# Optimization experiments

Hardware: AMD Instinct MI355X
Metric: run time of the kernel (lower is better)

The kernel has to match this reference:

```python
import jax, jax.numpy as jnp
import numpy as np
from jax import lax

B, T, I, H = 128, 48, 128, 512


def setup_inputs() -> dict:
    key = jax.random.key(0)
    ks = jax.random.split(key, 16)
    s = lambda *sh: 1.0 / np.sqrt(sh[-1])
    inp = {
        "decoder_x": jax.random.normal(ks[0], (B, T, I), jnp.float32),
        "x": jax.random.normal(ks[1], (B, T, 3), jnp.float32),
        # xavier_normal for [num_layers=1, B, H] -> std = sqrt(2/(B+H))
        "h0": jax.random.normal(ks[2], (B, H), jnp.float32) * np.sqrt(2.0 / (B + H)),
        "W1": jax.random.normal(ks[3], (H, H), jnp.float32) * s(H),
        "b1": jnp.zeros((H,), jnp.float32),
        "W2": jax.random.normal(ks[4], (H, I), jnp.float32) * s(I),
        "b2": jnp.zeros((H,), jnp.float32),
        "W3": jax.random.normal(ks[5], (1, H), jnp.float32) * s(H),
        "b3": jnp.zeros((1,), jnp.float32),
        "W4": jax.random.normal(ks[6], (H, I + 3), jnp.float32) * s(I + 3),
        "b4": jnp.zeros((H,), jnp.float32),
        "W_ih": jax.random.normal(ks[7], (3 * H, H), jnp.float32) * s(H),
        "W_hh": jax.random.normal(ks[8], (3 * H, H), jnp.float32) * s(H),
        "b_ih": jnp.zeros((3 * H,), jnp.float32),
        "b_hh": jnp.zeros((3 * H,), jnp.float32),
        "Wfc": jax.random.normal(ks[9], (1, H), jnp.float32) * s(H),
        "bfc": jnp.zeros((1,), jnp.float32),
    }
    return inp


def reference(decoder_x, x, h0, W1, b1, W2, b2, W3, b3, W4, b4,
              W_ih, W_hh, b_ih, b_hh, Wfc, bfc):
    Bc, Tc, Ic = decoder_x.shape
    # layer2(decoder_x) is step-invariant: compute once. [B, T, H]
    w2 = jnp.einsum('bti,hi->bth', decoder_x, W2) + b2

    def step(carry, x_t):
        h, _ = carry  # h: [B, H]
        w1 = h @ W1.T + b1                              # [B, H]
        # attention energies over the T_1 encoder window
        e = jnp.tanh(w1[:, None, :] + w2) @ W3[0] + b3[0]   # [B, T]
        a = jax.nn.softmax(e, axis=1)                   # [B, T]
        c = jnp.einsum('bti,bt->bi', decoder_x, a)      # weighted context [B, I]
        y0 = jnp.concatenate([c, x_t], axis=1) @ W4.T + b4  # [B, H]
        # single-step GRU (PyTorch gate order r, z, n)
        gi = y0 @ W_ih.T + b_ih
        gh = h @ W_hh.T + b_hh
        ir, iz, in_ = jnp.split(gi, 3, axis=1)
        hr, hz, hn = jnp.split(gh, 3, axis=1)
        r = jax.nn.sigmoid(ir + hr)
        z = jax.nn.sigmoid(iz + hz)
        n = jnp.tanh(in_ + r * hn)
        h_new = (1.0 - z) * n + z * h
        return (h_new, a), None

    xs = jnp.swapaxes(x, 0, 1)  # [T, B, 3]
    (h_f, a_f), _ = lax.scan(step, (h0, jnp.zeros((Bc, Tc), decoder_x.dtype)), xs)
    re = h_f @ Wfc.T + bfc      # fc(final_output[:, -1, :])  -> [B, 1]
    return re, a_f[:, :, None]  # weighted_alpha from last step [B, T, 1]
```

## Files before the change

### kernel.cpp

```cpp
#include <hip/hip_runtime.h>


typedef _Float16 half8 __attribute__((ext_vector_type(8)));
typedef _Float16 h2v  __attribute__((ext_vector_type(2)));
typedef float    f32x4 __attribute__((ext_vector_type(4)));
typedef unsigned int u32x3 __attribute__((ext_vector_type(3)));

#define OFF_BAR   0u
#define OFF_BZ    32768u
#define OFF_BC    40960u
#define OFF_WZ    65536u
#define OFF_WCT   2162688u
#define OFF_W2H   3178496u
#define OFF_HGH   9732096u
#define OFF_ZG    9863168u
#define OFF_DW    10911744u

__device__ __forceinline__ float fexp2(float x) { return __builtin_amdgcn_exp2f(x); }
__device__ __forceinline__ float frcp(float x)  { return __builtin_amdgcn_rcpf(x); }
__device__ __forceinline__ float fast_tanh(float x) {
  x = fminf(fmaxf(x, -15.f), 15.f);
  float e = fexp2(x * 2.8853900817779268f);
  return (e - 1.f) * frcp(e + 1.f);
}
__device__ __forceinline__ float fast_sigmoid(float x) {
  x = fminf(fmaxf(x, -30.f), 30.f);
  float e = fexp2(x * 1.4426950408889634f);
  return e * frcp(e + 1.f);
}

__device__ __forceinline__ void st_f32(float* p, float v) {
  __hip_atomic_store(p, v, __ATOMIC_RELAXED, __HIP_MEMORY_SCOPE_AGENT);
}
__device__ __forceinline__ unsigned long long ld_u64(const void* p) {
  return __hip_atomic_load((const unsigned long long*)p, __ATOMIC_RELAXED,
                           __HIP_MEMORY_SCOPE_AGENT);
}
__device__ __forceinline__ void st_u32(unsigned int* p, unsigned int v) {
  __hip_atomic_store(p, v, __ATOMIC_RELAXED, __HIP_MEMORY_SCOPE_AGENT);
}
union U2 { unsigned long long u; float f[2]; };
union H4 { unsigned long long u; _Float16 h[4]; };
union HU { unsigned int u; h2v h; };

__device__ __forceinline__ void poll_ge(unsigned int* fp, bool active,
                                        unsigned int target) {
  for (;;) {
    unsigned int v = active
      ? __hip_atomic_load(fp, __ATOMIC_RELAXED, __HIP_MEMORY_SCOPE_AGENT)
      : target;
    if (__ballot(v < target) == 0) break;
    __builtin_amdgcn_s_sleep(1);
  }
  __asm__ __volatile__("" ::: "memory");
}

__global__ __launch_bounds__(256) void prep_all(
    const float* __restrict__ dx, const float* __restrict__ h0,
    const float* __restrict__ W1, const float* __restrict__ Whh,
    const float* __restrict__ b1, const float* __restrict__ bhh,
    const float* __restrict__ Wih, const float* __restrict__ W4,
    const float* __restrict__ b4, const float* __restrict__ bih,
    const float* __restrict__ W2, const float* __restrict__ b2,
    _Float16* __restrict__ hgh,
    _Float16* __restrict__ Wzh, float* __restrict__ bz,
    float* __restrict__ bc, _Float16* __restrict__ WcT,
    _Float16* __restrict__ w2h, unsigned int* __restrict__ bar)
{
  __shared__ __align__(16) char smem[58368];
  const int bid = blockIdx.x;
  const int tid = threadIdx.x;
  const int lane = tid & 63, wv = tid >> 6;

  if (bid == 0) {
    for (int i = tid; i < 8192; i += 256) bar[i] = 0u;
  } else if (bid == 1) {
    for (int n = tid; n < 2048; n += 256)
      bz[n] = (n < 512) ? b1[n] : bhh[n - 512];
  } else if (bid < 18) {
    const int o0 = (bid - 2) * 96 + wv * 24;
    for (int it = 0; it < 24; ++it) {
      const int row = o0 + it;
      const float* r = Wih + row * 512 + lane * 8;
      float s = 0.f;
#pragma unroll
      for (int u = 0; u < 8; ++u) s += r[u] * b4[lane * 8 + u];
#pragma unroll
      for (int off = 32; off >= 1; off >>= 1) s += __shfl_xor(s, off);
      if (lane == 0) bc[row] = bih[row] + s;
    }
  } else if (bid < 34) {
    const int i0 = (bid - 18) * 4096 + tid * 16;
#pragma unroll
    for (int u = 0; u < 4; ++u) {
      float4 v = *(const float4*)(h0 + i0 + u * 4);
      H4 p; p.h[0] = (_Float16)v.x; p.h[1] = (_Float16)v.y;
      p.h[2] = (_Float16)v.z; p.h[3] = (_Float16)v.w;
      *(unsigned long long*)(hgh + i0 + u * 4) = p.u;
    }
  } else if (bid < 98) {
    const int i0 = (bid - 34) * 16384 + tid * 64;
#pragma unroll 4
    for (int u = 0; u < 16; ++u) {
      const int i = i0 + u * 4;
      const float* src = (i < 262144) ? (W1 + i) : (Whh + i - 262144);
      float4 v = *(const float4*)src;
      H4 p; p.h[0] = (_Float16)v.x; p.h[1] = (_Float16)v.y;
      p.h[2] = (_Float16)v.z; p.h[3] = (_Float16)v.w;
      *(unsigned long long*)(Wzh + i) = p.u;
    }
  } else if (bid < 194) {
    float* wih = (float*)smem;
    float* w4s = (float*)(smem + 4224);
    const int o0 = (bid - 98) * 16;
    const int k = tid;
    float acc[16];
#pragma unroll
    for (int i = 0; i < 16; ++i) acc[i] = 0.f;
    for (int jc = 0; jc < 512; jc += 64) {
      __syncthreads();
      for (int idx = tid; idx < 16 * 64; idx += 256) {
        int oo = idx >> 6, jj = idx & 63;
        wih[oo * 66 + jj] = Wih[(o0 + oo) * 512 + jc + jj];
      }
      for (int idx = tid; idx < 64 * 131; idx += 256) {
        int r = idx / 131, c = idx - r * 131;
        w4s[r * 132 + c] = W4[(jc + r) * 131 + c];
      }
      __syncthreads();
      if (k < 131) {
        for (int jj = 0; jj < 64; ++jj) {
          float w4v = w4s[jj * 132 + k];
#pragma unroll
          for (int oo = 0; oo < 16; ++oo) acc[oo] += wih[oo * 66 + jj] * w4v;
        }
      }
    }
    if (k < 131) {
#pragma unroll
      for (int oo = 0; oo < 16; ++oo)
        WcT[k * 1536 + o0 + oo] = (_Float16)acc[oo];
    }
  } else {
    float* dxa = (float*)smem;
    _Float16* w2t = (_Float16*)(smem + 24576);
    const int b = bid - 194;
    for (int idx = tid; idx < 48 * 128; idx += 256)
      dxa[idx] = dx[b * 6144 + idx];
    for (int hc = 0; hc < 4; ++hc) {
      __syncthreads();
      for (int idx = tid; idx < 128 * 128; idx += 256) {
        int hl = idx >> 7, i = idx & 127;
        w2t[i * 132 + hl] = (_Float16)W2[(hc * 128 + hl) * 128 + i];
      }
      __syncthreads();
      const int hh = tid & 127;
      const int tq = tid >> 7;
      const float b2v = b2[hc * 128 + hh];
      for (int tt = tq * 24; tt < tq * 24 + 24; ++tt) {
        float acc = b2v;
#pragma unroll 4
        for (int i = 0; i < 128; ++i)
          acc += dxa[tt * 128 + i] * (float)w2t[i * 132 + hh];
        w2h[(b * 48 + tt) * 512 + hc * 128 + hh] = (_Float16)acc;
      }
    }
  }
}

__global__ __launch_bounds__(256) void prep_dw(
    const float* __restrict__ dx, const _Float16* __restrict__ WcT,
    unsigned int* __restrict__ DW12)
{
  __shared__ float dxu[16 * 128];
  const int j = blockIdx.x;
  const int tid = threadIdx.x;
  const int u0 = j * 16;
  const float4* src = (const float4*)(dx + (size_t)u0 * 128);
  float4* dst4 = (float4*)dxu;
  for (int i = tid; i < 512; i += 256) dst4[i] = src[i];
  __syncthreads();
  const int c0 = tid * 2;
  float acc[16][6];
#pragma unroll
  for (int u = 0; u < 16; ++u)
#pragma unroll
    for (int g = 0; g < 6; ++g) acc[u][g] = 0.f;
  for (int k = 0; k < 128; ++k) {
    const _Float16* wr = WcT + k * 1536 + c0;
    h2v w0 = *(const h2v*)(wr);
    h2v w1v = *(const h2v*)(wr + 512);
    h2v w2v = *(const h2v*)(wr + 1024);
    const float f0 = (float)w0[0],  f1 = (float)w0[1];
    const float f2 = (float)w1v[0], f3 = (float)w1v[1];
    const float f4 = (float)w2v[0], f5 = (float)w2v[1];
#pragma unroll
    for (int u = 0; u < 16; ++u) {
      const float d = dxu[u * 128 + k];
      acc[u][0] += d * f0; acc[u][1] += d * f1; acc[u][2] += d * f2;
      acc[u][3] += d * f3; acc[u][4] += d * f4; acc[u][5] += d * f5;
    }
  }
#pragma unroll
  for (int u = 0; u < 16; ++u) {
    unsigned int* o = DW12 + (size_t)(u0 + u) * 768 + tid * 3;
    HU p;
    p.h[0] = (_Float16)acc[u][0]; p.h[1] = (_Float16)acc[u][1]; o[0] = p.u;
    p.h[0] = (_Float16)acc[u][2]; p.h[1] = (_Float16)acc[u][3]; o[1] = p.u;
    p.h[0] = (_Float16)acc[u][4]; p.h[1] = (_Float16)acc[u][5]; o[2] = p.u;
  }
}

#define DW_STEP(TB, CUR)                                                     \
  do {                                                                       \
    _Pragma("unroll")                                                        \
    for (int j = 0; j < 4; ++j) {                                            \
      const float a = asx[(TB) * 4 + j];                                     \
      HU p0, p1, p2; p0.u = CUR[j].x; p1.u = CUR[j].y; p2.u = CUR[j].z;      \
      aR0 += a * (float)p0.h[0]; aR1 += a * (float)p0.h[1];                  \
      aZ0 += a * (float)p1.h[0]; aZ1 += a * (float)p1.h[1];                  \
      aN0 += a * (float)p2.h[0]; aN1 += a * (float)p2.h[1];                  \
    }                                                                        \
    if ((TB) < 9) {                                                          \
      _Pragma("unroll")                                                      \
      for (int j = 0; j < 4; ++j)                                            \
        CUR[j] = *(const u32x3*)(dwp + (size_t)(((TB) + 3) * 4 + j) * 768);  \
    }                                                                        \
  } while (0)

__global__ __launch_bounds__(256, 1) void decoder_main(
    const float* __restrict__ xin, const float* __restrict__ h0,
    const float* __restrict__ W3, const float* __restrict__ b3,
    const float* __restrict__ Wfc, const float* __restrict__ bfc,
    const _Float16* __restrict__ Wzh, const float* __restrict__ bz,
    const _Float16* __restrict__ WcT, const float* __restrict__ bc,
    const _Float16* __restrict__ w2h, const unsigned int* __restrict__ DW12,
    _Float16* __restrict__ hgh, float* __restrict__ zg,
    unsigned int* __restrict__ bar, float* __restrict__ out)
{
  const int tid  = threadIdx.x;
  const int lane = tid & 63;
  const int wv   = tid >> 6;
  const int bid  = blockIdx.x;
  const int grp  = bid & 7;
  const int mem  = bid >> 3;
  const int b0   = grp * 16;
  const int myrow = b0 + mem;
  const int cb   = mem * 128;
  const int myIdx = grp * 16 + mem;
  const int base16 = grp * 16;
  unsigned int* zflag = bar;
  unsigned int* hflag = bar + 4096;

  __shared__ __align__(16) _Float16 w2lds[48 * 512];
  __shared__ __align__(16) char hlds[16384];
  __shared__ __align__(16) unsigned int dwlds[24 * 768];
  __shared__ float xlds[48 * 4];
  __shared__ float wfcs[512];
  __shared__ float es[48];
  __shared__ float asx[48];
  __shared__ float red[4];

  const int m = lane & 15, q = lane >> 4;

  half8 wzf[2][16];
  int   ncol[2];
  float bzv[2];
#pragma unroll
  for (int t = 0; t < 2; ++t) {
    ncol[t] = cb + (wv * 2 + t) * 16 + m;
    const _Float16* wrow = Wzh + ncol[t] * 512 + q * 8;
#pragma unroll
    for (int ks = 0; ks < 16; ++ks)
      wzf[t][ks] = *(const half8*)(wrow + ks * 32);
    bzv[t] = bz[ncol[t]];
  }
  float w3r[8];
#pragma unroll
  for (int u = 0; u < 8; ++u) w3r[u] = W3[lane * 8 + u];
  const float b3v  = b3[0];
  const float bfcv = bfc[0];

  const int c0 = tid * 2;
  const float bcR0 = bc[c0],        bcR1 = bc[c0 + 1];
  const float bcZ0 = bc[512 + c0],  bcZ1 = bc[513 + c0];
  const float bcN0 = bc[1024 + c0], bcN1 = bc[1025 + c0];
  float wxR[3][2], wxZ[3][2], wxN[3][2];
#pragma unroll
  for (int j2 = 0; j2 < 3; ++j2) {
    const _Float16* wr = WcT + (128 + j2) * 1536 + c0;
    wxR[j2][0] = (float)wr[0];    wxR[j2][1] = (float)wr[1];
    wxZ[j2][0] = (float)wr[512];  wxZ[j2][1] = (float)wr[513];
    wxN[j2][0] = (float)wr[1024]; wxN[j2][1] = (float)wr[1025];
  }
  float hA = h0[myrow * 512 + c0];
  float hB = h0[myrow * 512 + c0 + 1];

  const float* __restrict__ zrow = zg + (size_t)myrow * 2048;
  const unsigned int* __restrict__ dwp =
      DW12 + (size_t)myrow * 48 * 768 + (size_t)tid * 3;

  {
    const half8* w2src = (const half8*)(w2h + (size_t)myrow * 48 * 512);
    half8* w2dst = (half8*)w2lds;
    for (int i = tid; i < 3072; i += 256) w2dst[i] = w2src[i];
    for (int i = tid; i < 512; i += 256) wfcs[i] = Wfc[i];
    for (int i = tid; i < 144; i += 256) {
      const int t = i / 3, j2 = i - t * 3;
      xlds[t * 4 + j2] = xin[myrow * 144 + i];
    }
    const unsigned int* dwsrc = DW12 + (size_t)myrow * 48 * 768;
    for (int i = tid; i < 24 * 256; i += 256) {
      u32x3 v = *(const u32x3*)(dwsrc + (size_t)i * 3);
      *(u32x3*)(dwlds + (size_t)i * 3) = v;
    }
  }
  __syncthreads();

  for (int step = 0; step < 48; ++step) {
    {
      poll_ge(hflag + (size_t)(b0 + wv * 4 + (lane & 3)) * 32, lane < 4,
              (unsigned int)step);
      unsigned long long hv[8];
      const char* hbase = (const char*)hgh + (size_t)b0 * 1024 + (size_t)wv * 4096;
#pragma unroll
      for (int u = 0; u < 8; ++u)
        hv[u] = ld_u64(hbase + (size_t)(u * 64 + lane) * 8);
#pragma unroll
      for (int u = 0; u < 8; ++u) {
        const int n = wv * 512 + u * 64 + lane;
        const int row = n >> 7, b8 = (n & 127) * 8;
        *(unsigned long long*)(hlds + row * 1024 + (b8 ^ ((row & 7) << 4))) = hv[u];
      }
    }
    __syncthreads();

    {
      half8 af[16];
      const char* hb = hlds + m * 1024;
      const int sw = (m & 7) << 4;
#pragma unroll
      for (int ks = 0; ks < 16; ++ks)
        af[ks] = *(const half8*)(hb + ((ks * 64 + q * 16) ^ sw));
#pragma unroll
      for (int t = 0; t < 2; ++t) {
        f32x4 acc = {bzv[t], bzv[t], bzv[t], bzv[t]};
#pragma unroll
        for (int ks = 0; ks < 16; ++ks)
          acc = __builtin_amdgcn_mfma_f32_16x16x32_f16(af[ks], wzf[t][ks], acc, 0, 0, 0);
#pragma unroll
        for (int r = 0; r < 4; ++r)
          st_f32(&zg[(size_t)(b0 + q * 4 + r) * 2048 + ncol[t]], acc[r]);
      }
    }
    __syncthreads();
    if (tid == 0) st_u32(&zflag[(size_t)myIdx * 32], (unsigned int)(step + 1));

    poll_ge(zflag + (size_t)(base16 + (lane & 15)) * 32, lane < 16,
            (unsigned int)(step + 1));

    float w1r[8];
    {
#pragma unroll
      for (int u2 = 0; u2 < 4; ++u2) {
        U2 t2; t2.u = ld_u64(zrow + lane * 8 + u2 * 2);
        w1r[u2 * 2] = t2.f[0]; w1r[u2 * 2 + 1] = t2.f[1];
      }
    }
    U2 tr, tz, tn2;
    tr.u  = ld_u64(zrow + 512 + c0);
    tz.u  = ld_u64(zrow + 1024 + c0);
    tn2.u = ld_u64(zrow + 1536 + c0);
    u32x3 bA[4], bB[4], bC[4];
#pragma unroll
    for (int j = 0; j < 4; ++j) bA[j] = *(const u32x3*)(dwp + (size_t)(24 + j) * 768);
#pragma unroll
    for (int j = 0; j < 4; ++j) bB[j] = *(const u32x3*)(dwp + (size_t)(28 + j) * 768);
#pragma unroll
    for (int j = 0; j < 4; ++j) bC[j] = *(const u32x3*)(dwp + (size_t)(32 + j) * 768);

    {
      for (int tt = 0; tt < 12; ++tt) {
        const int t = wv * 12 + tt;
        half8 w2v = *(const half8*)(w2lds + t * 512 + lane * 8);
        float p = 0.f;
#pragma unroll
        for (int u = 0; u < 8; ++u)
          p += w3r[u] * fast_tanh(w1r[u] + (float)w2v[u]);
#pragma unroll
        for (int off = 32; off >= 1; off >>= 1) p += __shfl_xor(p, off);
        if (lane == 0) es[t] = p + b3v;
      }
      __syncthreads();
      if (wv == 0) {
        float e = (lane < 48) ? es[lane] : -1e30f;
        float mx = e;
#pragma unroll
        for (int off = 32; off >= 1; off >>= 1) mx = fmaxf(mx, __shfl_xor(mx, off));
        float pe = (lane < 48) ? fexp2((e - mx) * 1.4426950408889634f) : 0.f;
        float s = pe;
#pragma unroll
        for (int off = 32; off >= 1; off >>= 1) s += __shfl_xor(s, off);
        float a = pe * frcp(s);
        if (lane < 48) {
          asx[lane] = a;
          if (step == 47) out[128 + myrow * 48 + lane] = a;
        }
      }
      __syncthreads();
    }

    {
      float aR0 = bcR0, aR1 = bcR1, aZ0 = bcZ0, aZ1 = bcZ1, aN0 = bcN0, aN1 = bcN1;
#pragma unroll 4
      for (int t = 0; t < 24; ++t) {
        const float a = asx[t];
        u32x3 d = *(const u32x3*)(dwlds + (size_t)(t * 256 + tid) * 3);
        HU p0, p1, p2; p0.u = d.x; p1.u = d.y; p2.u = d.z;
        aR0 += a * (float)p0.h[0]; aR1 += a * (float)p0.h[1];
        aZ0 += a * (float)p1.h[0]; aZ1 += a * (float)p1.h[1];
        aN0 += a * (float)p2.h[0]; aN1 += a * (float)p2.h[1];
      }
      DW_STEP(6, bA);  DW_STEP(7, bB);  DW_STEP(8, bC);
      DW_STEP(9, bA);  DW_STEP(10, bB); DW_STEP(11, bC);

      const float x0 = xlds[step * 4], x1 = xlds[step * 4 + 1], x2 = xlds[step * 4 + 2];
      aR0 += x0 * wxR[0][0] + x1 * wxR[1][0] + x2 * wxR[2][0];
      aR1 += x0 * wxR[0][1] + x1 * wxR[1][1] + x2 * wxR[2][1];
      aZ0 += x0 * wxZ[0][0] + x1 * wxZ[1][0] + x2 * wxZ[2][0];
      aZ1 += x0 * wxZ[0][1] + x1 * wxZ[1][1] + x2 * wxZ[2][1];
      aN0 += x0 * wxN[0][0] + x1 * wxN[1][0] + x2 * wxN[2][0];
      aN1 += x0 * wxN[0][1] + x1 * wxN[1][1] + x2 * wxN[2][1];

      const float r0 = fast_sigmoid(aR0 + tr.f[0]), r1 = fast_sigmoid(aR1 + tr.f[1]);
      const float z0 = fast_sigmoid(aZ0 + tz.f[0]), z1 = fast_sigmoid(aZ1 + tz.f[1]);
      const float n0 = fast_tanh(aN0 + r0 * tn2.f[0]), n1 = fast_tanh(aN1 + r1 * tn2.f[1]);
      hA = (1.f - z0) * n0 + z0 * hA;
      hB = (1.f - z1) * n1 + z1 * hB;
      HU hp; hp.h[0] = (_Float16)hA; hp.h[1] = (_Float16)hB;
      st_u32((unsigned int*)(hgh + myrow * 512 + c0), hp.u);
    }
    __syncthreads();
    if (tid == 0) st_u32(&hflag[(size_t)myrow * 32], (unsigned int)(step + 1));
  }

  {
    float p = hA * wfcs[c0] + hB * wfcs[c0 + 1];
#pragma unroll
    for (int off = 32; off >= 1; off >>= 1) p += __shfl_xor(p, off);
    if (lane == 0) red[wv] = p;
    __syncthreads();
    if (tid == 0) out[myrow] = red[0] + red[1] + red[2] + red[3] + bfcv;
  }
}

extern "C" void kernel_launch(void* const* d_in, const int* in_sizes, int n_in,
                              void* d_out, int out_size, void* d_ws, size_t ws_size,
                              hipStream_t stream) {
  (void)in_sizes; (void)n_in; (void)out_size; (void)ws_size;
  const float* dx  = (const float*)d_in[0];
  const float* xin = (const float*)d_in[1];
  const float* h0  = (const float*)d_in[2];
  const float* W1  = (const float*)d_in[3];
  const float* b1  = (const float*)d_in[4];
  const float* W2  = (const float*)d_in[5];
  const float* b2  = (const float*)d_in[6];
  const float* W3  = (const float*)d_in[7];
  const float* b3  = (const float*)d_in[8];
  const float* W4  = (const float*)d_in[9];
  const float* b4  = (const float*)d_in[10];
  const float* Wih = (const float*)d_in[11];
  const float* Whh = (const float*)d_in[12];
  const float* bih = (const float*)d_in[13];
  const float* bhh = (const float*)d_in[14];
  const float* Wfc = (const float*)d_in[15];
  const float* bfc = (const float*)d_in[16];

  char* ws = (char*)d_ws;
  unsigned int* bar = (unsigned int*)(ws + OFF_BAR);
  float*     bz  = (float*)(ws + OFF_BZ);
  float*     bc  = (float*)(ws + OFF_BC);
  _Float16*  Wzh = (_Float16*)(ws + OFF_WZ);
  _Float16*  WcT = (_Float16*)(ws + OFF_WCT);
  _Float16*  w2h = (_Float16*)(ws + OFF_W2H);
  _Float16*  hgh = (_Float16*)(ws + OFF_HGH);
  float*     zg  = (float*)(ws + OFF_ZG);
  unsigned int* DW12 = (unsigned int*)(ws + OFF_DW);

  prep_all<<<322, 256, 0, stream>>>(dx, h0, W1, Whh, b1, bhh, Wih, W4, b4, bih,
                                    W2, b2, hgh, Wzh, bz, bc, WcT, w2h, bar);
  prep_dw<<<384, 256, 0, stream>>>(dx, WcT, DW12);
  decoder_main<<<128, 256, 0, stream>>>(xin, h0, W3, b3, Wfc, bfc,
                                        Wzh, bz, WcT, bc, w2h, DW12,
                                        hgh, zg, bar, (float*)d_out);
}
```

Before: 882.6 us.

## Use sc0 inline-asm loads and stores for inter-block flag and state exchange

After: 1.188 ms. +34.6%, slower.

```diff
diff --git a/kernel.cpp b/kernel.cpp
--- a/kernel.cpp
+++ b/kernel.cpp
@@ -43,12 +43,39 @@
 union H4 { unsigned long long u; _Float16 h[4]; };
 union HU { unsigned int u; h2v h; };
 
+__device__ __forceinline__ unsigned int ld_flag_sc0(const unsigned int* p) {
+  unsigned int v;
+  asm volatile("global_load_dword %0, %1, off sc0\n\t"
+               "s_waitcnt vmcnt(0)"
+               : "=v"(v) : "v"(p) : "memory");
+  return v;
+}
+__device__ __forceinline__ void st_u32_sc0(unsigned int* p, unsigned int v) {
+  asm volatile("global_store_dword %0, %1, off sc0" :: "v"(p), "v"(v) : "memory");
+}
+__device__ __forceinline__ void st_f32_sc0(float* p, float v) {
+  asm volatile("global_store_dword %0, %1, off sc0" :: "v"(p), "v"(v) : "memory");
+}
+__device__ __forceinline__ void drain_vm() {
+  asm volatile("s_waitcnt vmcnt(0)" ::: "memory");
+  __builtin_amdgcn_sched_barrier(0);
+}
+
 __device__ __forceinline__ void poll_ge(unsigned int* fp, bool active,
                                         unsigned int target) {
   for (;;) {
     unsigned int v = active
       ? __hip_atomic_load(fp, __ATOMIC_RELAXED, __HIP_MEMORY_SCOPE_AGENT)
       : target;
+    if (__ballot(v < target) == 0) break;
+    __builtin_amdgcn_s_sleep(1);
+  }
+  __asm__ __volatile__("" ::: "memory");
+}
+__device__ __forceinline__ void poll_ge_sc0(const unsigned int* fp,
+                                            unsigned int target) {
+  for (;;) {
+    unsigned int v = ld_flag_sc0(fp);
     if (__ballot(v < target) == 0) break;
     __builtin_amdgcn_s_sleep(1);
   }
@@ -260,8 +287,41 @@
   __shared__ float es[48];
   __shared__ float asx[48];
   __shared__ float red[4];
+  __shared__ unsigned int probe_sh;
 
   const int m = lane & 15, q = lane >> 4;
+
+  bool fast;
+  {
+    if (wv == 0) {
+      bool okr[2];
+#pragma unroll
+      for (int r = 1; r <= 2; ++r) {
+        if (lane == 0)
+          st_u32_sc0(zflag + (size_t)myIdx * 32 + 16, (unsigned int)r);
+        const unsigned int* pp = zflag + (size_t)(base16 + (lane & 15)) * 32 + 16;
+        bool ok = false;
+        for (int it = 0; it < 1000 && !ok; ++it) {
+          unsigned int v = ld_flag_sc0(pp);
+          if (__ballot(v < (unsigned int)r) == 0) ok = true;
+          else __builtin_amdgcn_s_sleep(8);
+        }
+        if (lane == 0)
+          st_u32(zflag + (size_t)myIdx * 32 + 16 + r, ok ? 2u : 1u);
+        unsigned int* vp = zflag + (size_t)(base16 + (lane & 15)) * 32 + 16 + r;
+        unsigned int v;
+        for (;;) {
+          v = __hip_atomic_load(vp, __ATOMIC_RELAXED, __HIP_MEMORY_SCOPE_AGENT);
+          if (__ballot(v == 0u) == 0) break;
+          __builtin_amdgcn_s_sleep(1);
+        }
+        okr[r - 1] = (__ballot(v == 2u) == ~0ull);
+      }
+      if (lane == 0) probe_sh = (okr[0] && okr[1]) ? 1u : 0u;
+    }
+    __syncthreads();
+    fast = (probe_sh != 0u);
+  }
 
   half8 wzf[2][16];
   int   ncol[2];
@@ -319,18 +379,42 @@
 
   for (int step = 0; step < 48; ++step) {
     {
-      poll_ge(hflag + (size_t)(b0 + wv * 4 + (lane & 3)) * 32, lane < 4,
-              (unsigned int)step);
-      unsigned long long hv[8];
-      const char* hbase = (const char*)hgh + (size_t)b0 * 1024 + (size_t)wv * 4096;
-#pragma unroll
-      for (int u = 0; u < 8; ++u)
-        hv[u] = ld_u64(hbase + (size_t)(u * 64 + lane) * 8);
-#pragma unroll
-      for (int u = 0; u < 8; ++u) {
-        const int n = wv * 512 + u * 64 + lane;
-        const int row = n >> 7, b8 = (n & 127) * 8;
-        *(unsigned long long*)(hlds + row * 1024 + (b8 ^ ((row & 7) << 4))) = hv[u];
+      if (fast) {
+        poll_ge_sc0(hflag + (size_t)(b0 + wv * 4 + (lane & 3)) * 32,
+                    (unsigned int)step);
+        f32x4 hv4[4];
+        const char* ab = (const char*)hgh + (size_t)b0 * 1024 +
+                         (size_t)wv * 4096 + (size_t)lane * 16;
+        asm volatile(
+          "global_load_dwordx4 %0, %4, off sc0\n\t"
+          "global_load_dwordx4 %1, %4, off offset:1024 sc0\n\t"
+          "global_load_dwordx4 %2, %4, off offset:2048 sc0\n\t"
+          "global_load_dwordx4 %3, %4, off offset:3072 sc0\n\t"
+          "s_waitcnt vmcnt(0)"
+          : "=v"(hv4[0]), "=v"(hv4[1]), "=v"(hv4[2]), "=v"(hv4[3])
+          : "v"(ab) : "memory");
+#pragma unroll
+        for (int v2 = 0; v2 < 4; ++v2) {
+          const int c = v2 * 64 + lane;
+          const int n0 = wv * 512 + c * 2;
+          const int row = n0 >> 7;
+          const int x = (n0 & 127) * 8;
+          *(f32x4*)(hlds + row * 1024 + (x ^ ((row & 7) << 4))) = hv4[v2];
+        }
+      } else {
+        poll_ge(hflag + (size_t)(b0 + wv * 4 + (lane & 3)) * 32, lane < 4,
+                (unsigned int)step);
+        unsigned long long hv[8];
+        const char* hbase = (const char*)hgh + (size_t)b0 * 1024 + (size_t)wv * 4096;
+#pragma unroll
+        for (int u = 0; u < 8; ++u)
+          hv[u] = ld_u64(hbase + (size_t)(u * 64 + lane) * 8);
+#pragma unroll
+        for (int u = 0; u < 8; ++u) {
+          const int n = wv * 512 + u * 64 + lane;
+          const int row = n >> 7, b8 = (n & 127) * 8;
+          *(unsigned long long*)(hlds + row * 1024 + (b8 ^ ((row & 7) << 4))) = hv[u];
+        }
       }
     }
     __syncthreads();
@@ -348,29 +432,61 @@
 #pragma unroll
         for (int ks = 0; ks < 16; ++ks)
           acc = __builtin_amdgcn_mfma_f32_16x16x32_f16(af[ks], wzf[t][ks], acc, 0, 0, 0);
-#pragma unroll
-        for (int r = 0; r < 4; ++r)
-          st_f32(&zg[(size_t)(b0 + q * 4 + r) * 2048 + ncol[t]], acc[r]);
-      }
-    }
+        if (fast) {
+#pragma unroll
+          for (int r = 0; r < 4; ++r)
+            st_f32_sc0(&zg[(size_t)(b0 + q * 4 + r) * 2048 + ncol[t]], acc[r]);
+        } else {
+#pragma unroll
+          for (int r = 0; r < 4; ++r)
+            st_f32(&zg[(size_t)(b0 + q * 4 + r) * 2048 + ncol[t]], acc[r]);
+        }
+      }
+    }
+    if (fast) drain_vm();
     __syncthreads();
-    if (tid == 0) st_u32(&zflag[(size_t)myIdx * 32], (unsigned int)(step + 1));
-
-    poll_ge(zflag + (size_t)(base16 + (lane & 15)) * 32, lane < 16,
-            (unsigned int)(step + 1));
+    if (tid == 0) {
+      if (fast) st_u32_sc0(&zflag[(size_t)myIdx * 32], (unsigned int)(step + 1));
+      else      st_u32(&zflag[(size_t)myIdx * 32], (unsigned int)(step + 1));
+    }
+
+    if (fast)
+      poll_ge_sc0(zflag + (size_t)(base16 + (lane & 15)) * 32,
+                  (unsigned int)(step + 1));
+    else
+      poll_ge(zflag + (size_t)(base16 + (lane & 15)) * 32, lane < 16,
+              (unsigned int)(step + 1));
 
     float w1r[8];
-    {
+    U2 tr, tz, tn2;
+    if (fast) {
+      f32x4 za, zb;
+      const float* wp = zrow + lane * 8;
+      asm volatile(
+        "global_load_dwordx4 %0, %2, off sc0\n\t"
+        "global_load_dwordx4 %1, %2, off offset:16 sc0\n\t"
+        "s_waitcnt vmcnt(0)"
+        : "=v"(za), "=v"(zb) : "v"(wp) : "memory");
+      __builtin_amdgcn_sched_barrier(0);
+      w1r[0] = za[0]; w1r[1] = za[1]; w1r[2] = za[2]; w1r[3] = za[3];
+      w1r[4] = zb[0]; w1r[5] = zb[1]; w1r[6] = zb[2]; w1r[7] = zb[3];
+      asm volatile(
+        "global_load_dwordx2 %0, %3, off sc0\n\t"
+        "global_load_dwordx2 %1, %4, off sc0\n\t"
+        "global_load_dwordx2 %2, %5, off sc0"
+        : "=v"(tr.u), "=v"(tz.u), "=v"(tn2.u)
+        : "v"(zrow + 512 + c0), "v"(zrow + 1024 + c0), "v"(zrow + 1536 + c0)
+        : "memory");
+    } else {
 #pragma unroll
       for (int u2 = 0; u2 < 4; ++u2) {
         U2 t2; t2.u = ld_u64(zrow + lane * 8 + u2 * 2);
         w1r[u2 * 2] = t2.f[0]; w1r[u2 * 2 + 1] = t2.f[1];
       }
-    }
-    U2 tr, tz, tn2;
-    tr.u  = ld_u64(zrow + 512 + c0);
-    tz.u  = ld_u64(zrow + 1024 + c0);
-    tn2.u = ld_u64(zrow + 1536 + c0);
+      tr.u  = ld_u64(zrow + 512 + c0);
+      tz.u  = ld_u64(zrow + 1024 + c0);
+      tn2.u = ld_u64(zrow + 1536 + c0);
+    }
     u32x3 bA[4], bB[4], bC[4];
 #pragma unroll
     for (int j = 0; j < 4; ++j) bA[j] = *(const u32x3*)(dwp + (size_t)(24 + j) * 768);
@@ -432,16 +548,22 @@
       aN0 += x0 * wxN[0][0] + x1 * wxN[1][0] + x2 * wxN[2][0];
       aN1 += x0 * wxN[0][1] + x1 * wxN[1][1] + x2 * wxN[2][1];
 
+      if (fast) drain_vm();
       const float r0 = fast_sigmoid(aR0 + tr.f[0]), r1 = fast_sigmoid(aR1 + tr.f[1]);
       const float z0 = fast_sigmoid(aZ0 + tz.f[0]), z1 = fast_sigmoid(aZ1 + tz.f[1]);
       const float n0 = fast_tanh(aN0 + r0 * tn2.f[0]), n1 = fast_tanh(aN1 + r1 * tn2.f[1]);
       hA = (1.f - z0) * n0 + z0 * hA;
       hB = (1.f - z1) * n1 + z1 * hB;
       HU hp; hp.h[0] = (_Float16)hA; hp.h[1] = (_Float16)hB;
-      st_u32((unsigned int*)(hgh + myrow * 512 + c0), hp.u);
-    }
+      if (fast) st_u32_sc0((unsigned int*)(hgh + myrow * 512 + c0), hp.u);
+      else      st_u32((unsigned int*)(hgh + myrow * 512 + c0), hp.u);
+    }
+    if (fast) drain_vm();
     __syncthreads();
-    if (tid == 0) st_u32(&hflag[(size_t)myrow * 32], (unsigned int)(step + 1));
+    if (tid == 0) {
+      if (fast) st_u32_sc0(&hflag[(size_t)myrow * 32], (unsigned int)(step + 1));
+      else      st_u32(&hflag[(size_t)myrow * 32], (unsigned int)(step + 1));
+    }
   }
 
   {
```

## Double decoder block to 512 threads, splitting MFMA and attention work across 8 waves

Applied to the files above, without the earlier changes.

Result: faster. 846.4 us (-4.1%).

```diff
diff --git a/kernel.cpp b/kernel.cpp
--- a/kernel.cpp
+++ b/kernel.cpp
@@ -228,7 +228,7 @@
     }                                                                        \
   } while (0)
 
-__global__ __launch_bounds__(256, 1) void decoder_main(
+__global__ __launch_bounds__(512, 2) void decoder_main(
     const float* __restrict__ xin, const float* __restrict__ h0,
     const float* __restrict__ W3, const float* __restrict__ b3,
     const float* __restrict__ Wfc, const float* __restrict__ bfc,
@@ -263,25 +263,23 @@
 
   const int m = lane & 15, q = lane >> 4;
 
-  half8 wzf[2][16];
-  int   ncol[2];
-  float bzv[2];
-#pragma unroll
-  for (int t = 0; t < 2; ++t) {
-    ncol[t] = cb + (wv * 2 + t) * 16 + m;
-    const _Float16* wrow = Wzh + ncol[t] * 512 + q * 8;
+  half8 wzf[16];
+  const int ncol = cb + wv * 16 + m;
+  {
+    const _Float16* wrow = Wzh + ncol * 512 + q * 8;
 #pragma unroll
     for (int ks = 0; ks < 16; ++ks)
-      wzf[t][ks] = *(const half8*)(wrow + ks * 32);
-    bzv[t] = bz[ncol[t]];
-  }
+      wzf[ks] = *(const half8*)(wrow + ks * 32);
+  }
+  const float bzv = bz[ncol];
   float w3r[8];
 #pragma unroll
   for (int u = 0; u < 8; ++u) w3r[u] = W3[lane * 8 + u];
   const float b3v  = b3[0];
   const float bfcv = bfc[0];
 
-  const int c0 = tid * 2;
+  const int t2 = tid & 255;
+  const int c0 = t2 * 2;
   const float bcR0 = bc[c0],        bcR1 = bc[c0 + 1];
   const float bcZ0 = bc[512 + c0],  bcZ1 = bc[513 + c0];
   const float bcN0 = bc[1024 + c0], bcN1 = bc[1025 + c0];
@@ -298,19 +296,19 @@
 
   const float* __restrict__ zrow = zg + (size_t)myrow * 2048;
   const unsigned int* __restrict__ dwp =
-      DW12 + (size_t)myrow * 48 * 768 + (size_t)tid * 3;
+      DW12 + (size_t)myrow * 48 * 768 + (size_t)t2 * 3;
 
   {
     const half8* w2src = (const half8*)(w2h + (size_t)myrow * 48 * 512);
     half8* w2dst = (half8*)w2lds;
-    for (int i = tid; i < 3072; i += 256) w2dst[i] = w2src[i];
-    for (int i = tid; i < 512; i += 256) wfcs[i] = Wfc[i];
-    for (int i = tid; i < 144; i += 256) {
+    for (int i = tid; i < 3072; i += 512) w2dst[i] = w2src[i];
+    for (int i = tid; i < 512; i += 512) wfcs[i] = Wfc[i];
+    for (int i = tid; i < 144; i += 512) {
       const int t = i / 3, j2 = i - t * 3;
       xlds[t * 4 + j2] = xin[myrow * 144 + i];
     }
     const unsigned int* dwsrc = DW12 + (size_t)myrow * 48 * 768;
-    for (int i = tid; i < 24 * 256; i += 256) {
+    for (int i = tid; i < 24 * 256; i += 512) {
       u32x3 v = *(const u32x3*)(dwsrc + (size_t)i * 3);
       *(u32x3*)(dwlds + (size_t)i * 3) = v;
     }
@@ -318,17 +316,19 @@
   __syncthreads();
 
   for (int step = 0; step < 48; ++step) {
+    if (wv == 0)
+      poll_ge(hflag + (size_t)(b0 + (lane & 15)) * 32, lane < 16,
+              (unsigned int)step);
+    __syncthreads();
     {
-      poll_ge(hflag + (size_t)(b0 + wv * 4 + (lane & 3)) * 32, lane < 4,
-              (unsigned int)step);
-      unsigned long long hv[8];
-      const char* hbase = (const char*)hgh + (size_t)b0 * 1024 + (size_t)wv * 4096;
-#pragma unroll
-      for (int u = 0; u < 8; ++u)
+      unsigned long long hv[4];
+      const char* hbase = (const char*)hgh + (size_t)b0 * 1024 + (size_t)wv * 2048;
+#pragma unroll
+      for (int u = 0; u < 4; ++u)
         hv[u] = ld_u64(hbase + (size_t)(u * 64 + lane) * 8);
 #pragma unroll
-      for (int u = 0; u < 8; ++u) {
-        const int n = wv * 512 + u * 64 + lane;
+      for (int u = 0; u < 4; ++u) {
+        const int n = wv * 256 + u * 64 + lane;
         const int row = n >> 7, b8 = (n & 127) * 8;
         *(unsigned long long*)(hlds + row * 1024 + (b8 ^ ((row & 7) << 4))) = hv[u];
       }
@@ -342,46 +342,45 @@
 #pragma unroll
       for (int ks = 0; ks < 16; ++ks)
         af[ks] = *(const half8*)(hb + ((ks * 64 + q * 16) ^ sw));
-#pragma unroll
-      for (int t = 0; t < 2; ++t) {
-        f32x4 acc = {bzv[t], bzv[t], bzv[t], bzv[t]};
-#pragma unroll
-        for (int ks = 0; ks < 16; ++ks)
-          acc = __builtin_amdgcn_mfma_f32_16x16x32_f16(af[ks], wzf[t][ks], acc, 0, 0, 0);
-#pragma unroll
-        for (int r = 0; r < 4; ++r)
-          st_f32(&zg[(size_t)(b0 + q * 4 + r) * 2048 + ncol[t]], acc[r]);
-      }
+      f32x4 acc = {bzv, bzv, bzv, bzv};
+#pragma unroll
+      for (int ks = 0; ks < 16; ++ks)
+        acc = __builtin_amdgcn_mfma_f32_16x16x32_f16(af[ks], wzf[ks], acc, 0, 0, 0);
+#pragma unroll
+      for (int r = 0; r < 4; ++r)
+        st_f32(&zg[(size_t)(b0 + q * 4 + r) * 2048 + ncol], acc[r]);
     }
     __syncthreads();
     if (tid == 0) st_u32(&zflag[(size_t)myIdx * 32], (unsigned int)(step + 1));
 
-    poll_ge(zflag + (size_t)(base16 + (lane & 15)) * 32, lane < 16,
-            (unsigned int)(step + 1));
+    if (wv == 0)
+      poll_ge(zflag + (size_t)(base16 + (lane & 15)) * 32, lane < 16,
+              (unsigned int)(step + 1));
+    __syncthreads();
 
     float w1r[8];
+#pragma unroll
+    for (int u2 = 0; u2 < 4; ++u2) {
+      U2 t2u; t2u.u = ld_u64(zrow + lane * 8 + u2 * 2);
+      w1r[u2 * 2] = t2u.f[0]; w1r[u2 * 2 + 1] = t2u.f[1];
+    }
+    U2 tr, tz, tn2;
+    u32x3 bA[4], bB[4], bC[4];
+    if (tid < 256) {
+      tr.u  = ld_u64(zrow + 512 + c0);
+      tz.u  = ld_u64(zrow + 1024 + c0);
+      tn2.u = ld_u64(zrow + 1536 + c0);
+#pragma unroll
+      for (int j = 0; j < 4; ++j) bA[j] = *(const u32x3*)(dwp + (size_t)(24 + j) * 768);
+#pragma unroll
+      for (int j = 0; j < 4; ++j) bB[j] = *(const u32x3*)(dwp + (size_t)(28 + j) * 768);
+#pragma unroll
+      for (int j = 0; j < 4; ++j) bC[j] = *(const u32x3*)(dwp + (size_t)(32 + j) * 768);
+    }
+
     {
-#pragma unroll
-      for (int u2 = 0; u2 < 4; ++u2) {
-        U2 t2; t2.u = ld_u64(zrow + lane * 8 + u2 * 2);
-        w1r[u2 * 2] = t2.f[0]; w1r[u2 * 2 + 1] = t2.f[1];
-      }
-    }
-    U2 tr, tz, tn2;
-    tr.u  = ld_u64(zrow + 512 + c0);
-    tz.u  = ld_u64(zrow + 1024 + c0);
-    tn2.u = ld_u64(zrow + 1536 + c0);
-    u32x3 bA[4], bB[4], bC[4];
-#pragma unroll
-    for (int j = 0; j < 4; ++j) bA[j] = *(const u32x3*)(dwp + (size_t)(24 + j) * 768);
-#pragma unroll
-    for (int j = 0; j < 4; ++j) bB[j] = *(const u32x3*)(dwp + (size_t)(28 + j) * 768);
-#pragma unroll
-    for (int j = 0; j < 4; ++j) bC[j] = *(const u32x3*)(dwp + (size_t)(32 + j) * 768);
-
-    {
-      for (int tt = 0; tt < 12; ++tt) {
-        const int t = wv * 12 + tt;
+      for (int tt = 0; tt < 6; ++tt) {
+        const int t = wv * 6 + tt;
         half8 w2v = *(const half8*)(w2lds + t * 512 + lane * 8);
         float p = 0.f;
 #pragma unroll
@@ -410,12 +409,12 @@
       __syncthreads();
     }
 
-    {
+    if (tid < 256) {
       float aR0 = bcR0, aR1 = bcR1, aZ0 = bcZ0, aZ1 = bcZ1, aN0 = bcN0, aN1 = bcN1;
 #pragma unroll 4
       for (int t = 0; t < 24; ++t) {
         const float a = asx[t];
-        u32x3 d = *(const u32x3*)(dwlds + (size_t)(t * 256 + tid) * 3);
+        u32x3 d = *(const u32x3*)(dwlds + (size_t)(t * 256 + t2) * 3);
         HU p0, p1, p2; p0.u = d.x; p1.u = d.y; p2.u = d.z;
         aR0 += a * (float)p0.h[0]; aR1 += a * (float)p0.h[1];
         aZ0 += a * (float)p1.h[0]; aZ1 += a * (float)p1.h[1];
@@ -444,14 +443,14 @@
     if (tid == 0) st_u32(&hflag[(size_t)myrow * 32], (unsigned int)(step + 1));
   }
 
-  {
+  if (tid < 256) {
     float p = hA * wfcs[c0] + hB * wfcs[c0 + 1];
 #pragma unroll
     for (int off = 32; off >= 1; off >>= 1) p += __shfl_xor(p, off);
     if (lane == 0) red[wv] = p;
-    __syncthreads();
-    if (tid == 0) out[myrow] = red[0] + red[1] + red[2] + red[3] + bfcv;
-  }
+  }
+  __syncthreads();
+  if (tid == 0) out[myrow] = red[0] + red[1] + red[2] + red[3] + bfcv;
 }
 
 extern "C" void kernel_launch(void* const* d_in, const int* in_sizes, int n_in,
@@ -490,7 +489,7 @@
   prep_all<<<322, 256, 0, stream>>>(dx, h0, W1, Whh, b1, bhh, Wih, W4, b4, bih,
                                     W2, b2, hgh, Wzh, bz, bc, WcT, w2h, bar);
   prep_dw<<<384, 256, 0, stream>>>(dx, WcT, DW12);
-  decoder_main<<<128, 256, 0, stream>>>(xin, h0, W3, b3, Wfc, bfc,
+  decoder_main<<<128, 512, 0, stream>>>(xin, h0, W3, b3, Wfc, bfc,
                                         Wzh, bz, WcT, bc, w2h, DW12,
                                         hgh, zg, bar, (float*)d_out);
 }
```
